# Optimization experiments

Hardware: AMD Instinct MI355X
Metric: run time of the kernel (lower is better)

The kernel has to match this reference:

```python
import jax, jax.numpy as jnp
import numpy as np

N, T, C, H = 512, 64, 64, 4
HD = C // H
FE = 4  # forward_expansion
EPS = 1e-5


def _p(key, shape, scale=0.05):
    return jax.random.normal(key, shape, dtype=jnp.float32) * scale


def setup_inputs() -> dict:
    key = jax.random.key(0)
    ks = jax.random.split(key, 24)
    return {
        'value': jax.random.normal(ks[0], (N, T, C), dtype=jnp.float32),
        'key_t': jax.random.normal(ks[1], (N, T, C), dtype=jnp.float32),
        'query': jax.random.normal(ks[2], (N, T, C), dtype=jnp.float32),
        'adj': jax.random.uniform(ks[3], (N, N), dtype=jnp.float32),
        # SSelfAttention params (nn.Linear weights, applied as x @ W.T)
        'Wv': _p(ks[4], (HD, HD)), 'Wk': _p(ks[5], (HD, HD)), 'Wq': _p(ks[6], (HD, HD)),
        'Wo': _p(ks[7], (C, C)), 'bo': jnp.zeros((C,), jnp.float32),
        # LayerNorms
        'g1': jnp.ones((C,), jnp.float32), 'b1': jnp.zeros((C,), jnp.float32),
        'g2': jnp.ones((C,), jnp.float32), 'b2': jnp.zeros((C,), jnp.float32),
        # FFN
        'Wf1': _p(ks[8], (FE * C, C)), 'bf1': jnp.zeros((FE * C,), jnp.float32),
        'Wf2': _p(ks[9], (C, FE * C)), 'bf2': jnp.zeros((C,), jnp.float32),
        # GCN (two GraphConvolution layers: adj @ (x @ W) + b, ReLU between)
        'Wg1': _p(ks[10], (C, C)), 'bg1': jnp.zeros((C,), jnp.float32),
        'Wg2': _p(ks[11], (C, C)), 'bg2': jnp.zeros((C,), jnp.float32),
        # gating linears
        'Wo1': _p(ks[12], (C, C)), 'bo1': jnp.zeros((C,), jnp.float32),
        'Wo2': _p(ks[13], (C, C)), 'bo2': jnp.zeros((C,), jnp.float32),
    }


def _layernorm(x, g, b):
    m = jnp.mean(x, axis=-1, keepdims=True)
    v = jnp.mean((x - m) ** 2, axis=-1, keepdims=True)
    return (x - m) * jax.lax.rsqrt(v + EPS) * g + b


def reference(value, key_t, query, adj, Wv, Wk, Wq, Wo, bo, g1, b1, g2, b2,
              Wf1, bf1, Wf2, bf2, Wg1, bg1, Wg2, bg2, Wo1, bo1, Wo2, bo2):
    n, t, c = query.shape
    # --- SSelfAttention: attention across nodes (q/k axes are nodes) ---
    vh = value.reshape(n, t, H, HD) @ Wv.T
    kh = key_t.reshape(n, t, H, HD) @ Wk.T
    qh = query.reshape(n, t, H, HD) @ Wq.T
    energy = jnp.einsum('qthd,kthd->qkth', qh, kh)  # [N,N,T,H]
    att = jax.nn.softmax(energy / jnp.sqrt(jnp.float32(c)), axis=1)
    attn_out = jnp.einsum('qkth,kthd->qthd', att, vh).reshape(n, t, c)
    attn_out = attn_out @ Wo.T + bo
    # --- residual + norm + FFN + norm (dropout = identity, eval mode) ---
    x = _layernorm(attn_out + query, g1, b1)
    ffn = jax.nn.relu(x @ Wf1.T + bf1) @ Wf2.T + bf2
    out1 = _layernorm(ffn + x, g2, b2)
    # --- InstanceNorm2d(1) on adj: normalize over whole NxN map (no affine) ---
    am = jnp.mean(adj)
    av = jnp.mean((adj - am) ** 2)
    adj_n = (adj - am) * jax.lax.rsqrt(av + EPS)
    # --- GCN applied per-timestep, vectorized over T ---
    h = jax.nn.relu(jnp.einsum('nm,mtc->ntc', adj_n, query @ Wg1.T) + bg1)
    out2 = jnp.einsum('nm,mtc->ntc', adj_n, h @ Wg2.T) + bg2
    # --- gated fusion ---
    g = jax.nn.sigmoid(out1 @ Wo1.T + bo1 + out2 @ Wo2.T + bo2)
    return g * out1 + (1.0 - g) * out2
```

## Files before the change

kernel.cpp:

```cpp
#include <hip/hip_runtime.h>

#define LN_EPS 1e-5f

typedef __attribute__((ext_vector_type(4))) short short4v;
typedef __attribute__((ext_vector_type(4))) float float4v;

__device__ __forceinline__ float wave_sum(float v) {
#pragma unroll
  for (int o = 32; o > 0; o >>= 1) v += __shfl_xor(v, o, 64);
  return v;
}

__device__ __forceinline__ unsigned short f2b(float f) {
  unsigned int u = __float_as_uint(f);
  u += 0x7fffu + ((u >> 16) & 1u);
  return (unsigned short)(u >> 16);
}

__device__ __forceinline__ float b2f(unsigned short h) {
  return __uint_as_float(((unsigned int)h) << 16);
}

__device__ __forceinline__ float4v mfma_16x16x16_bf16(short4v a, short4v b,
                                                      float4v c) {
#if __has_builtin(__builtin_amdgcn_mfma_f32_16x16x16bf16_1k)
  return __builtin_amdgcn_mfma_f32_16x16x16bf16_1k(a, b, c, 0, 0, 0);
#else
  float4v d;
  asm volatile(
      "v_mfma_f32_16x16x16_bf16 %0, %1, %2, %3\n\ts_nop 7\n\ts_nop 7"
      : "=v"(d)
      : "v"(a), "v"(b), "v"(c));
  return d;
#endif
}

__global__ __launch_bounds__(256) void s1_kernel(
    const float* __restrict__ adj, float* __restrict__ ps,
    float* __restrict__ pss, const float* __restrict__ value,
    const float* __restrict__ keyt, const float* __restrict__ query,
    const float* __restrict__ Wv, const float* __restrict__ Wk,
    const float* __restrict__ Wq, unsigned short* __restrict__ vt,
    unsigned short* __restrict__ kh, unsigned short* __restrict__ qh) {
  __shared__ float r1[4], r2[4];
  __shared__ __align__(16) float wv[256], wk[256], wq[256];
  const int b = blockIdx.x, tid = threadIdx.x;
  if (b < 512) {
    float v0 = adj[b * 512 + tid], v1 = adj[b * 512 + 256 + tid];
    float s = v0 + v1;
    float ss = fmaf(v0, v0, v1 * v1);
    s = wave_sum(s);
    ss = wave_sum(ss);
    if ((tid & 63) == 0) { r1[tid >> 6] = s; r2[tid >> 6] = ss; }
    __syncthreads();
    if (tid == 0) {
      ps[b] = r1[0] + r1[1] + r1[2] + r1[3];
      pss[b] = r2[0] + r2[1] + r2[2] + r2[3];
    }
  } else {
    wv[tid] = Wv[tid];
    wk[tid] = Wk[tid];
    wq[tid] = Wq[tid] * 0.125f;
    __syncthreads();
    const int th = b - 512;
    const int t = th >> 2, h = th & 3;
    const int base = t * 64 + h * 16;
    float y[16];
    unsigned short tmp[16];

#define XFORM(SRC, WARR)                                            \
  {                                                                 \
    const float4* p = (const float4*)(SRC + n * 4096 + base);       \
    float x[16];                                                    \
    *(float4*)(x + 0) = p[0];                                       \
    *(float4*)(x + 4) = p[1];                                       \
    *(float4*)(x + 8) = p[2];                                       \
    *(float4*)(x + 12) = p[3];                                      \
    _Pragma("unroll") for (int d = 0; d < 16; ++d) {                \
      float acc = 0.f;                                              \
      _Pragma("unroll") for (int e4 = 0; e4 < 4; ++e4) {            \
        float4 w4 = *(const float4*)&WARR[d * 16 + e4 * 4];         \
        acc = fmaf(w4.x, x[e4 * 4 + 0], acc);                       \
        acc = fmaf(w4.y, x[e4 * 4 + 1], acc);                       \
        acc = fmaf(w4.z, x[e4 * 4 + 2], acc);                       \
        acc = fmaf(w4.w, x[e4 * 4 + 3], acc);                       \
      }                                                             \
      y[d] = acc;                                                   \
    }                                                               \
  }

    for (int s = 0; s < 2; ++s) {
      const int n = tid + (s << 8);
      XFORM(value, wv)
#pragma unroll
      for (int d = 0; d < 16; ++d) vt[th * 8192 + d * 512 + n] = f2b(y[d]);
      XFORM(keyt, wk)
#pragma unroll
      for (int d = 0; d < 16; ++d) tmp[d] = f2b(y[d]);
      *(int4*)&kh[(th * 512 + n) * 16] = *(int4*)&tmp[0];
      *(int4*)&kh[(th * 512 + n) * 16 + 8] = *(int4*)&tmp[8];
      XFORM(query, wq)
#pragma unroll
      for (int d = 0; d < 16; ++d) tmp[d] = f2b(y[d]);
      *(int4*)&qh[(th * 512 + n) * 16] = *(int4*)&tmp[0];
      *(int4*)&qh[(th * 512 + n) * 16 + 8] = *(int4*)&tmp[8];
    }
#undef XFORM
  }
}

#define VPAD 536
__global__ __launch_bounds__(256) void s2_kernel(
    const float* __restrict__ adj, const float* __restrict__ ps,
    const float* __restrict__ pss, const float* __restrict__ query,
    const float* __restrict__ Wg1, const float* __restrict__ Wf1,
    const float* __restrict__ Wf2, const float* __restrict__ Wo1,
    const float* __restrict__ Wo2, const float* __restrict__ Wg2,
    const float* __restrict__ Wo, const float* __restrict__ bg2,
    const float* __restrict__ bo1, const float* __restrict__ bo2,
    unsigned short* __restrict__ anh, unsigned short* __restrict__ anl,
    unsigned short* __restrict__ Yfh, unsigned short* __restrict__ Yfl,
    unsigned short* __restrict__ Wf1f, unsigned short* __restrict__ Wf2f,
    unsigned short* __restrict__ Wo1f, unsigned short* __restrict__ Wg2hf,
    unsigned short* __restrict__ Wg2lf, unsigned short* __restrict__ W32hf,
    unsigned short* __restrict__ W32lf, unsigned short* __restrict__ Wof,
    float* __restrict__ c2, const unsigned short* __restrict__ qh,
    const unsigned short* __restrict__ kh, const unsigned short* __restrict__ vt,
    unsigned short* __restrict__ obf) {
  __shared__ float r1[4], r2[4];
  __shared__ __align__(16) char smem[33280];
  const int tid = threadIdx.x, b = blockIdx.x;
  if (b < 900) {
    float* pool = (float*)smem;
    if (b < 256) {
      float s = ps[tid] + ps[tid + 256];
      float ss = pss[tid] + pss[tid + 256];
      s = wave_sum(s);
      ss = wave_sum(ss);
      if ((tid & 63) == 0) { r1[tid >> 6] = s; r2[tid >> 6] = ss; }
      __syncthreads();
      const float sum = r1[0] + r1[1] + r1[2] + r1[3];
      const float sqs = r2[0] + r2[1] + r2[2] + r2[3];
      const float am = sum * (1.f / 262144.f);
      const float var = sqs * (1.f / 262144.f) - am * am;
      const float rs = rsqrtf(var + LN_EPS);
      const int i = (b * 256 + tid) * 4;
      float4 v = *(const float4*)&adj[i];
      float vals[4] = {(v.x - am) * rs, (v.y - am) * rs, (v.z - am) * rs,
                       (v.w - am) * rs};
      unsigned short th4[4], tl4[4];
#pragma unroll
      for (int j = 0; j < 4; ++j) {
        th4[j] = f2b(vals[j]);
        tl4[j] = f2b(vals[j] - b2f(th4[j]));
      }
      *(short4v*)&anh[i] = *(short4v*)th4;
      *(short4v*)&anl[i] = *(short4v*)tl4;
    } else if (b < 320) {
      const int id = (b - 256) * 256 + tid;
      const int n = id >> 6, k = id & 63;
      Wf1f[((k >> 4) * 256 + n) * 16 + (k & 15)] = f2b(Wf1[id]);
    } else if (b < 384) {
      const int id = (b - 320) * 256 + tid;
      const int n = id >> 8, k = id & 255;
      Wf2f[((k >> 4) * 64 + n) * 16 + (k & 15)] = f2b(Wf2[id]);
    } else if (b < 896) {
      const int pb = b - 384;
      const int w = tid >> 6, lane = tid & 63;
      const int mt = pb & 31;
      const int t = (pb >> 5) * 4 + w;
      float* xs = pool;
      float* Ls = pool + 256;
      float wc[64];
#pragma unroll
      for (int e = 0; e < 16; ++e)
        *(float4*)&wc[e * 4] = *(const float4*)&Wg1[lane * 64 + e * 4];
#pragma unroll 4
      for (int ms = 0; ms < 16; ++ms) {
        const int r = (mt * 16 + ms) * 64 + t;
        xs[w * 64 + lane] = query[r * 64 + lane];
        float acc = 0.f;
#pragma unroll
        for (int e = 0; e < 64; ++e) acc = fmaf(xs[w * 64 + e], wc[e], acc);
        Ls[(w * 16 + ms) * 68 + lane] = acc;
      }
      unsigned int dh[8], dl[8];
#pragma unroll
      for (int j = 0; j < 8; ++j) {
        float v0 = Ls[(w * 16 + 2 * j) * 68 + lane];
        float v1 = Ls[(w * 16 + 2 * j + 1) * 68 + lane];
        unsigned int h0 = f2b(v0), h1 = f2b(v1);
        unsigned int l0 = f2b(v0 - b2f((unsigned short)h0));
        unsigned int l1 = f2b(v1 - b2f((unsigned short)h1));
        dh[j] = h0 | (h1 << 16);
        dl[j] = l0 | (l1 << 16);
      }
      const int off = ((mt * 4096) + t * 64 + lane) * 16;
      *(uint4*)(Yfh + off) = *(uint4*)&dh[0];
      *(uint4*)(Yfh + off + 8) = *(uint4*)&dh[4];
      *(uint4*)(Yfl + off) = *(uint4*)&dl[0];
      *(uint4*)(Yfl + off + 8) = *(uint4*)&dl[4];
    } else if (b == 896) {
      for (int i = tid; i < 4096; i += 256) {
        const int n = i >> 6, k = i & 63;
        Wo1f[((k >> 4) * 64 + n) * 16 + (k & 15)] = f2b(Wo1[i]);
      }
    } else if (b == 897) {
      for (int i = tid; i < 4096; i += 256) {
        const int n = i >> 6, k = i & 63;
        const float v = Wg2[i];
        const unsigned short h = f2b(v);
        const unsigned short l = f2b(v - b2f(h));
        Wg2hf[((k >> 4) * 64 + n) * 16 + (k & 15)] = h;
        Wg2lf[((k >> 4) * 64 + n) * 16 + (k & 15)] = l;
      }
    } else if (b == 898) {
      float* wo2s = pool;
      float* wg2s = pool + 4096;
      float* bg2s = pool + 8192;
      for (int i = tid; i < 4096; i += 256) {
        wo2s[i] = Wo2[i];
        wg2s[i] = Wg2[i];
      }
      if (tid < 64) bg2s[tid] = bg2[tid];
      __syncthreads();
#pragma unroll 4
      for (int t = 0; t < 16; ++t) {
        const int i = t * 256 + tid;
        const int r = i >> 6, c = i & 63;
        float acc = 0.f;
#pragma unroll
        for (int e = 0; e < 64; ++e)
          acc = fmaf(wo2s[r * 64 + e], wg2s[e * 64 + c], acc);
        const unsigned short h = f2b(acc);
        const unsigned short l = f2b(acc - b2f(h));
        W32hf[((c >> 4) * 64 + r) * 16 + (c & 15)] = h;
        W32lf[((c >> 4) * 64 + r) * 16 + (c & 15)] = l;
      }
      if (tid < 64) {
        float acc = bo1[tid] + bo2[tid];
#pragma unroll
        for (int e = 0; e < 64; ++e)
          acc = fmaf(wo2s[tid * 64 + e], bg2s[e], acc);
        c2[tid] = acc;
      }
    } else {
      for (int i = tid; i < 4096; i += 256) {
        const int n = i >> 6, k = i & 63;
        Wof[((k >> 4) * 64 + n) * 16 + (k & 15)] = f2b(Wo[i]);
      }
    }
  } else {
    unsigned short* Vs = (unsigned short*)smem;
    const int bx = b - 900;
    const int th = bx >> 2;
    {
      const unsigned short* vb = vt + th * 8192;
#pragma unroll
      for (int it = 0; it < 4; ++it) {
        const int flat = (it * 256 + tid) * 8;
        const int d = flat >> 9, k = flat & 511;
        *(int4*)&Vs[d * VPAD + k] = *(const int4*)&vb[flat];
      }
    }
    __syncthreads();

    const int lane = tid & 15;
    const int quad = (tid >> 4) & 3;
    const int w = tid >> 6;
    const int q0 = (bx & 3) * 128 + w * 32;

    const unsigned short* qbase = qh + th * 8192;
    const unsigned short* kbase = kh + th * 8192;
    short4v qf[2];
#pragma unroll
    for (int ct = 0; ct < 2; ++ct)
      qf[ct] = *(const short4v*)&qbase[(q0 + ct * 16 + lane) * 16 + quad * 4];

    float4v acc[2];
    float l[2];
#pragma unroll
    for (int ct = 0; ct < 2; ++ct) {
      acc[ct].x = 0.f; acc[ct].y = 0.f; acc[ct].z = 0.f; acc[ct].w = 0.f;
      l[ct] = 0.f;
    }
    float4v zero;
    zero.x = 0.f; zero.y = 0.f; zero.z = 0.f; zero.w = 0.f;

    const unsigned short* vrow = &Vs[lane * VPAD];

    for (int kt = 0; kt < 32; ++kt) {
      const short4v kf =
          *(const short4v*)&kbase[(kt * 16 + lane) * 16 + quad * 4];
      const short4v vf = *(const short4v*)&vrow[kt * 16 + quad * 4];
#pragma unroll
      for (int ct = 0; ct < 2; ++ct) {
        float4v s = mfma_16x16x16_bf16(kf, qf[ct], zero);
        float p0 = __expf(s.x);
        float p1 = __expf(s.y);
        float p2 = __expf(s.z);
        float p3 = __expf(s.w);
        l[ct] += (p0 + p1) + (p2 + p3);
        unsigned int u0 = __float_as_uint(p0) + 0x8000u;
        unsigned int u1 = __float_as_uint(p1) + 0x8000u;
        unsigned int u2 = __float_as_uint(p2) + 0x8000u;
        unsigned int u3 = __float_as_uint(p3) + 0x8000u;
        union {
          uint2 u;
          short4v s4;
        } pk;
        pk.u.x = __builtin_amdgcn_perm(u1, u0, 0x07060302u);
        pk.u.y = __builtin_amdgcn_perm(u3, u2, 0x07060302u);
        acc[ct] = mfma_16x16x16_bf16(vf, pk.s4, acc[ct]);
      }
    }

    const int t = th >> 2, h = th & 3;
#pragma unroll
    for (int ct = 0; ct < 2; ++ct) {
      float lt = l[ct];
      lt += __shfl_xor(lt, 16, 64);
      lt += __shfl_xor(lt, 32, 64);
      const float inv = 1.f / lt;
      unsigned short tmp[4];
      tmp[0] = f2b(acc[ct].x * inv);
      tmp[1] = f2b(acc[ct].y * inv);
      tmp[2] = f2b(acc[ct].z * inv);
      tmp[3] = f2b(acc[ct].w * inv);
      const int q = q0 + ct * 16 + lane;
      *(uint2*)&obf[(q * 64 + t) * 64 + h * 16 + quad * 4] = *(uint2*)tmp;
    }
  }
}

__global__ __launch_bounds__(256) void s3_kernel(
    const unsigned short* __restrict__ obf, const float* __restrict__ query,
    const unsigned short* __restrict__ Wof, const float* __restrict__ bo,
    const float* __restrict__ g1, const float* __restrict__ b1,
    const unsigned short* __restrict__ Wf1f, const float* __restrict__ bf1,
    const unsigned short* __restrict__ Wf2f, const float* __restrict__ bf2,
    const float* __restrict__ g2, const float* __restrict__ b2,
    float* __restrict__ out1, unsigned short* __restrict__ out1b,
    const unsigned short* __restrict__ Ah, const unsigned short* __restrict__ Al,
    const unsigned short* __restrict__ Bh, const unsigned short* __restrict__ Bl,
    const float* __restrict__ bg1, unsigned short* __restrict__ Hh,
    unsigned short* __restrict__ Hl) {
  __shared__ __align__(16) char smem[41984];
  const int tid = threadIdx.x, b = blockIdx.x;
  const int w = tid >> 6, lane = tid & 63;
  const int ln = lane & 15, quad = lane >> 4;
  if (b < 512) {
    unsigned short* xb = (unsigned short*)smem;
    unsigned short* hid = (unsigned short*)(smem + 8704);
    const int n = b;
    float xres[4][4];

    {
      const unsigned short* ap = obf + (n * 64 + w * 16 + ln) * 64 + quad * 4;
      float4v acc[4];
#pragma unroll
      for (int j = 0; j < 4; ++j) {
        acc[j].x = 0.f; acc[j].y = 0.f; acc[j].z = 0.f; acc[j].w = 0.f;
      }
#pragma unroll
      for (int kt = 0; kt < 4; ++kt) {
        const short4v a = *(const short4v*)(ap + kt * 16);
#pragma unroll
        for (int j = 0; j < 4; ++j) {
          const short4v bfr =
              *(const short4v*)&Wof[(kt * 64 + j * 16 + ln) * 16 + quad * 4];
          acc[j] = mfma_16x16x16_bf16(a, bfr, acc[j]);
        }
      }
#pragma unroll
      for (int reg = 0; reg < 4; ++reg) {
        const int row = w * 16 + quad * 4 + reg;
        float v[4];
        float s = 0.f;
#pragma unroll
        for (int j = 0; j < 4; ++j) {
          const int col = j * 16 + ln;
          v[j] = acc[j][reg] + bo[col] + query[(n * 64 + row) * 64 + col];
          s += v[j];
        }
        s += __shfl_xor(s, 1, 64);
        s += __shfl_xor(s, 2, 64);
        s += __shfl_xor(s, 4, 64);
        s += __shfl_xor(s, 8, 64);
        const float mean = s * 0.015625f;
        float vv = 0.f;
#pragma unroll
        for (int j = 0; j < 4; ++j) {
          const float dd = v[j] - mean;
          vv += dd * dd;
        }
        vv += __shfl_xor(vv, 1, 64);
        vv += __shfl_xor(vv, 2, 64);
        vv += __shfl_xor(vv, 4, 64);
        vv += __shfl_xor(vv, 8, 64);
        const float rs = rsqrtf(vv * 0.015625f + LN_EPS);
#pragma unroll
        for (int j = 0; j < 4; ++j) {
          const int col = j * 16 + ln;
          const float xv = (v[j] - mean) * rs * g1[col] + b1[col];
          xres[j][reg] = xv;
          xb[row * 68 + col] = f2b(xv);
        }
      }
    }
    __syncthreads();

    {
      const int wm = (w & 1) * 32, wn = (w >> 1) * 128;
      float4v acc[2][8];
#pragma unroll
      for (int i = 0; i < 2; ++i)
#pragma unroll
        for (int j = 0; j < 8; ++j) {
          acc[i][j].x = 0.f; acc[i][j].y = 0.f;
          acc[i][j].z = 0.f; acc[i][j].w = 0.f;
        }
#pragma unroll
      for (int kt = 0; kt < 4; ++kt) {
        short4v a0 = *(const short4v*)&xb[(wm + ln) * 68 + kt * 16 + quad * 4];
        short4v a1 =
            *(const short4v*)&xb[(wm + 16 + ln) * 68 + kt * 16 + quad * 4];
#pragma unroll
        for (int j = 0; j < 8; ++j) {
          short4v bfr = *(const short4v*)&Wf1f[(kt * 256 + wn + j * 16 + ln) *
                                                   16 + quad * 4];
          acc[0][j] = mfma_16x16x16_bf16(a0, bfr, acc[0][j]);
          acc[1][j] = mfma_16x16x16_bf16(a1, bfr, acc[1][j]);
        }
      }
#pragma unroll
      for (int mt = 0; mt < 2; ++mt)
#pragma unroll
        for (int j = 0; j < 8; ++j) {
          const int col = wn + j * 16 + ln;
          const float bb = bf1[col];
#pragma unroll
          for (int reg = 0; reg < 4; ++reg) {
            const int row = wm + mt * 16 + quad * 4 + reg;
            hid[row * 260 + col] = f2b(fmaxf(acc[mt][j][reg] + bb, 0.f));
          }
        }
    }
    __syncthreads();

    {
      float4v acc[4];
#pragma unroll
      for (int j = 0; j < 4; ++j) {
        acc[j].x = 0.f; acc[j].y = 0.f; acc[j].z = 0.f; acc[j].w = 0.f;
      }
#pragma unroll 4
      for (int kt = 0; kt < 16; ++kt) {
        short4v a =
            *(const short4v*)&hid[(w * 16 + ln) * 260 + kt * 16 + quad * 4];
#pragma unroll
        for (int j = 0; j < 4; ++j) {
          short4v bfr =
              *(const short4v*)&Wf2f[(kt * 64 + j * 16 + ln) * 16 + quad * 4];
          acc[j] = mfma_16x16x16_bf16(a, bfr, acc[j]);
        }
      }
#pragma unroll
      for (int reg = 0; reg < 4; ++reg) {
        const int row = w * 16 + quad * 4 + reg;
        float v[4];
        float s = 0.f;
#pragma unroll
        for (int j = 0; j < 4; ++j) {
          v[j] = acc[j][reg] + bf2[j * 16 + ln] + xres[j][reg];
          s += v[j];
        }
        s += __shfl_xor(s, 1, 64);
        s += __shfl_xor(s, 2, 64);
        s += __shfl_xor(s, 4, 64);
        s += __shfl_xor(s, 8, 64);
        const float mean = s * 0.015625f;
        float vv = 0.f;
#pragma unroll
        for (int j = 0; j < 4; ++j) {
          const float dd = v[j] - mean;
          vv += dd * dd;
        }
        vv += __shfl_xor(vv, 1, 64);
        vv += __shfl_xor(vv, 2, 64);
        vv += __shfl_xor(vv, 4, 64);
        vv += __shfl_xor(vv, 8, 64);
        const float rs = rsqrtf(vv * 0.015625f + LN_EPS);
#pragma unroll
        for (int j = 0; j < 4; ++j) {
          const float ov =
              (v[j] - mean) * rs * g2[j * 16 + ln] + b2[j * 16 + ln];
          const int idx = (n * 64 + row) * 64 + j * 16 + ln;
          out1[idx] = ov;
          out1b[idx] = f2b(ov);
        }
      }
    }
  } else {
    const int pb = b - 512;
    const int wave = w;
    const int wm = (wave & 1) * 32, wn = (wave >> 1) * 64;
    const int m0 = (pb >> 5) * 64 + wm;
    const int n0 = (pb & 31) * 128 + wn;

    const unsigned short* ah0 = Ah + (m0 + ln) * 512 + quad * 4;
    const unsigned short* al0 = Al + (m0 + ln) * 512 + quad * 4;
    const unsigned short* bh0 = Bh + (n0 + ln) * 16 + quad * 4;
    const unsigned short* bl0 = Bl + (n0 + ln) * 16 + quad * 4;

    float4v acc[2][4];
#pragma unroll
    for (int i = 0; i < 2; ++i)
#pragma unroll
      for (int j = 0; j < 4; ++j) {
        acc[i][j].x = 0.f; acc[i][j].y = 0.f;
        acc[i][j].z = 0.f; acc[i][j].w = 0.f;
      }

#pragma unroll 2
    for (int kt = 0; kt < 32; ++kt) {
      short4v a0h = *(const short4v*)(ah0 + kt * 16);
      short4v a1h = *(const short4v*)(ah0 + 16 * 512 + kt * 16);
      short4v a0l = *(const short4v*)(al0 + kt * 16);
      short4v a1l = *(const short4v*)(al0 + 16 * 512 + kt * 16);
#pragma unroll
      for (int j = 0; j < 4; ++j) {
        const int boff = (kt * 4096 + j * 16) * 16;
        short4v bh = *(const short4v*)(bh0 + boff);
        short4v bl = *(const short4v*)(bl0 + boff);
        acc[0][j] = mfma_16x16x16_bf16(a0l, bh, acc[0][j]);
        acc[0][j] = mfma_16x16x16_bf16(a0h, bl, acc[0][j]);
        acc[0][j] = mfma_16x16x16_bf16(a0h, bh, acc[0][j]);
        acc[1][j] = mfma_16x16x16_bf16(a1l, bh, acc[1][j]);
        acc[1][j] = mfma_16x16x16_bf16(a1h, bl, acc[1][j]);
        acc[1][j] = mfma_16x16x16_bf16(a1h, bh, acc[1][j]);
      }
    }

#pragma unroll
    for (int mt = 0; mt < 2; ++mt) {
      const int mtile = (m0 + mt * 16) >> 4;
#pragma unroll
      for (int j = 0; j < 4; ++j) {
        const int col = n0 + j * 16 + ln;
        const float bb = bg1[col & 63];
        unsigned short hh[4], hl[4];
#pragma unroll
        for (int reg = 0; reg < 4; ++reg) {
          float v = fmaxf(acc[mt][j][reg] + bb, 0.f);
          hh[reg] = f2b(v);
          hl[reg] = f2b(v - b2f(hh[reg]));
        }
        const int off = (mtile * 4096 + col) * 16 + quad * 4;
        *(uint2*)&Hh[off] = *(uint2*)hh;
        *(uint2*)&Hl[off] = *(uint2*)hl;
      }
    }
  }
}

__global__ __launch_bounds__(256) void s4_kernel(
    const unsigned short* __restrict__ Ah, const unsigned short* __restrict__ Al,
    const unsigned short* __restrict__ Bh, const unsigned short* __restrict__ Bl,
    unsigned short* __restrict__ G2h, unsigned short* __restrict__ G2l) {
  const int tid = threadIdx.x;
  const int wave = tid >> 6, lane = tid & 63;
  const int ln = lane & 15, quad = lane >> 4;
  const int wm = (wave & 1) * 32, wn = (wave >> 1) * 32;
  const int m0 = (blockIdx.x >> 6) * 64 + wm;
  const int n0 = (blockIdx.x & 63) * 64 + wn;

  const unsigned short* ah0 = Ah + (m0 + ln) * 512 + quad * 4;
  const unsigned short* al0 = Al + (m0 + ln) * 512 + quad * 4;
  const unsigned short* bh0 = Bh + (n0 + ln) * 16 + quad * 4;
  const unsigned short* bl0 = Bl + (n0 + ln) * 16 + quad * 4;

  float4v acc[2][2];
#pragma unroll
  for (int i = 0; i < 2; ++i)
#pragma unroll
    for (int j = 0; j < 2; ++j) {
      acc[i][j].x = 0.f; acc[i][j].y = 0.f;
      acc[i][j].z = 0.f; acc[i][j].w = 0.f;
    }

#pragma unroll 4
  for (int kt = 0; kt < 32; ++kt) {
    short4v a0h = *(const short4v*)(ah0 + kt * 16);
    short4v a1h = *(const short4v*)(ah0 + 16 * 512 + kt * 16);
    short4v a0l = *(const short4v*)(al0 + kt * 16);
    short4v a1l = *(const short4v*)(al0 + 16 * 512 + kt * 16);
#pragma unroll
    for (int j = 0; j < 2; ++j) {
      const int boff = (kt * 4096 + j * 16) * 16;
      short4v bh = *(const short4v*)(bh0 + boff);
      short4v bl = *(const short4v*)(bl0 + boff);
      acc[0][j] = mfma_16x16x16_bf16(a0l, bh, acc[0][j]);
      acc[0][j] = mfma_16x16x16_bf16(a0h, bl, acc[0][j]);
      acc[0][j] = mfma_16x16x16_bf16(a0h, bh, acc[0][j]);
      acc[1][j] = mfma_16x16x16_bf16(a1l, bh, acc[1][j]);
      acc[1][j] = mfma_16x16x16_bf16(a1h, bl, acc[1][j]);
      acc[1][j] = mfma_16x16x16_bf16(a1h, bh, acc[1][j]);
    }
  }

#pragma unroll
  for (int mt = 0; mt < 2; ++mt)
#pragma unroll
    for (int j = 0; j < 2; ++j) {
      const int col = n0 + j * 16 + ln;
#pragma unroll
      for (int reg = 0; reg < 4; ++reg) {
        const int row = m0 + mt * 16 + quad * 4 + reg;
        const float v = acc[mt][j][reg];
        const unsigned short h = f2b(v);
        G2h[row * 4096 + col] = h;
        G2l[row * 4096 + col] = f2b(v - b2f(h));
      }
    }
}

__global__ __launch_bounds__(256) void s5_kernel(
    const unsigned short* __restrict__ out1b, const float* __restrict__ out1,
    const unsigned short* __restrict__ G2h, const unsigned short* __restrict__ G2l,
    const unsigned short* __restrict__ Wo1f, const unsigned short* __restrict__ Wg2hf,
    const unsigned short* __restrict__ Wg2lf, const unsigned short* __restrict__ W32hf,
    const unsigned short* __restrict__ W32lf, const float* __restrict__ bg2,
    const float* __restrict__ c2, float* __restrict__ dst) {
  const int tid = threadIdx.x;
  const int wave = tid >> 6, lane = tid & 63;
  const int ln = lane & 15, quad = lane >> 4;
  const int m0 = blockIdx.x * 64 + wave * 16;

  const unsigned short* o1p = out1b + (m0 + ln) * 64 + quad * 4;
  const unsigned short* ghp = G2h + (m0 + ln) * 64 + quad * 4;
  const unsigned short* glp = G2l + (m0 + ln) * 64 + quad * 4;

  float4v aco[4], aca[4];
#pragma unroll
  for (int j = 0; j < 4; ++j) {
    aco[j].x = 0.f; aco[j].y = 0.f; aco[j].z = 0.f; aco[j].w = 0.f;
    aca[j].x = 0.f; aca[j].y = 0.f; aca[j].z = 0.f; aca[j].w = 0.f;
  }

#pragma unroll
  for (int kt = 0; kt < 4; ++kt) {
    const short4v ao = *(const short4v*)(o1p + kt * 16);
    const short4v gh = *(const short4v*)(ghp + kt * 16);
    const short4v gl = *(const short4v*)(glp + kt * 16);
#pragma unroll
    for (int j = 0; j < 4; ++j) {
      const int boff = (kt * 64 + j * 16 + ln) * 16 + quad * 4;
      const short4v wgh = *(const short4v*)(Wg2hf + boff);
      const short4v wgl = *(const short4v*)(Wg2lf + boff);
      const short4v wo1 = *(const short4v*)(Wo1f + boff);
      const short4v w3h = *(const short4v*)(W32hf + boff);
      const short4v w3l = *(const short4v*)(W32lf + boff);
      aco[j] = mfma_16x16x16_bf16(gl, wgh, aco[j]);
      aco[j] = mfma_16x16x16_bf16(gh, wgl, aco[j]);
      aco[j] = mfma_16x16x16_bf16(gh, wgh, aco[j]);
      aca[j] = mfma_16x16x16_bf16(ao, wo1, aca[j]);
      aca[j] = mfma_16x16x16_bf16(gl, w3h, aca[j]);
      aca[j] = mfma_16x16x16_bf16(gh, w3l, aca[j]);
      aca[j] = mfma_16x16x16_bf16(gh, w3h, aca[j]);
    }
  }

#pragma unroll
  for (int j = 0; j < 4; ++j) {
    const int col = j * 16 + ln;
    const float bg2v = bg2[col];
    const float c2v = c2[col];
#pragma unroll
    for (int reg = 0; reg < 4; ++reg) {
      const int row = m0 + quad * 4 + reg;
      const float o2 = aco[j][reg] + bg2v;
      const float a = aca[j][reg] + c2v;
      const float o1v = out1[row * 64 + col];
      const float g = 1.f / (1.f + __expf(-a));
      dst[row * 64 + col] = o2 + g * (o1v - o2);
    }
  }
}

extern "C" void kernel_launch(void* const* d_in, const int* in_sizes, int n_in,
                              void* d_out, int out_size, void* d_ws,
                              size_t ws_size, hipStream_t stream) {
  const float* value = (const float*)d_in[0];
  const float* key_t = (const float*)d_in[1];
  const float* query = (const float*)d_in[2];
  const float* adj = (const float*)d_in[3];
  const float* Wv = (const float*)d_in[4];
  const float* Wk = (const float*)d_in[5];
  const float* Wq = (const float*)d_in[6];
  const float* Wo = (const float*)d_in[7];
  const float* bo = (const float*)d_in[8];
  const float* g1 = (const float*)d_in[9];
  const float* b1 = (const float*)d_in[10];
  const float* g2 = (const float*)d_in[11];
  const float* b2 = (const float*)d_in[12];
  const float* Wf1 = (const float*)d_in[13];
  const float* bf1 = (const float*)d_in[14];
  const float* Wf2 = (const float*)d_in[15];
  const float* bf2 = (const float*)d_in[16];
  const float* Wg1 = (const float*)d_in[17];
  const float* bg1 = (const float*)d_in[18];
  const float* Wg2 = (const float*)d_in[19];
  const float* bg2 = (const float*)d_in[20];
  const float* Wo1 = (const float*)d_in[21];
  const float* bo1 = (const float*)d_in[22];
  const float* Wo2 = (const float*)d_in[23];
  const float* bo2 = (const float*)d_in[24];

  float* ws = (float*)d_ws;
  const size_t M1 = 1048576;
  unsigned short* obf = (unsigned short*)(ws + 0);
  float* out1 = ws + 2 * M1;
  unsigned short* out1b = (unsigned short*)(ws + 4 * M1);
  unsigned short* qh = (unsigned short*)(ws + 5 * M1);
  unsigned short* kh = (unsigned short*)(ws + 6 * M1);
  unsigned short* vt = (unsigned short*)(ws + 7 * M1);
  unsigned short* Yfh = (unsigned short*)(ws + 8 * M1);
  unsigned short* Yfl = (unsigned short*)(ws + 9 * M1);
  unsigned short* Hrfh = (unsigned short*)(ws + 10 * M1);
  unsigned short* Hrfl = (unsigned short*)(ws + 11 * M1);
  unsigned short* G2h = (unsigned short*)(ws + 12 * M1);
  unsigned short* G2l = (unsigned short*)(ws + 13 * M1);
  unsigned short* anh = (unsigned short*)(ws + 14 * M1);
  unsigned short* anl = (unsigned short*)(ws + 14 * M1 + 131072);
  float* wbase = ws + 14 * M1 + 262144;
  unsigned short* Wf1f = (unsigned short*)(wbase);
  unsigned short* Wf2f = (unsigned short*)(wbase + 8192);
  unsigned short* Wo1f = (unsigned short*)(wbase + 16384);
  unsigned short* Wg2hf = (unsigned short*)(wbase + 18432);
  unsigned short* Wg2lf = (unsigned short*)(wbase + 20480);
  unsigned short* W32hf = (unsigned short*)(wbase + 22528);
  unsigned short* W32lf = (unsigned short*)(wbase + 24576);
  unsigned short* Wof = (unsigned short*)(wbase + 26624);
  float* c2 = wbase + 28672;
  float* ps = wbase + 28736;
  float* pss = ps + 512;
  float* dst = (float*)d_out;

  s1_kernel<<<768, 256, 0, stream>>>(adj, ps, pss, value, key_t, query, Wv,
                                     Wk, Wq, vt, kh, qh);
  s2_kernel<<<1924, 256, 0, stream>>>(adj, ps, pss, query, Wg1, Wf1, Wf2, Wo1,
                                      Wo2, Wg2, Wo, bg2, bo1, bo2, anh, anl,
                                      Yfh, Yfl, Wf1f, Wf2f, Wo1f, Wg2hf,
                                      Wg2lf, W32hf, W32lf, Wof, c2, qh, kh,
                                      vt, obf);
  s3_kernel<<<768, 256, 0, stream>>>(obf, query, Wof, bo, g1, b1, Wf1f, bf1,
                                     Wf2f, bf2, g2, b2, out1, out1b, anh, anl,
                                     Yfh, Yfl, bg1, Hrfh, Hrfl);
  s4_kernel<<<512, 256, 0, stream>>>(anh, anl, Hrfh, Hrfl, G2h, G2l);
  s5_kernel<<<512, 256, 0, stream>>>(out1b, out1, G2h, G2l, Wo1f, Wg2hf,
                                     Wg2lf, W32hf, W32lf, bg2, c2, dst);
}
```

Before: 253.0 us.

## Fuse GCN second aggregation with gated-fusion epilogue through shared memory

Merges the adjacency-aggregation GEMM (s4) and the gating/output kernel (s5) into one kernel. The aggregated tile stays in LDS instead of being written to global memory as hi/lo bf16 pairs and read back, which also removes one launch. The three split-precision products now go into separate accumulators so the MFMA chains are independent, at the cost of more registers. Each block now covers one timestep for 64 nodes, so the out1/dst accesses are strided by timestep.

```diff
diff --git a/kernel.cpp b/kernel.cpp
--- a/kernel.cpp
+++ b/kernel.cpp
@@ -564,126 +564,134 @@
   }
 }
 
-__global__ __launch_bounds__(256) void s4_kernel(
+__global__ __launch_bounds__(256) void s45_kernel(
     const unsigned short* __restrict__ Ah, const unsigned short* __restrict__ Al,
     const unsigned short* __restrict__ Bh, const unsigned short* __restrict__ Bl,
-    unsigned short* __restrict__ G2h, unsigned short* __restrict__ G2l) {
-  const int tid = threadIdx.x;
-  const int wave = tid >> 6, lane = tid & 63;
-  const int ln = lane & 15, quad = lane >> 4;
-  const int wm = (wave & 1) * 32, wn = (wave >> 1) * 32;
-  const int m0 = (blockIdx.x >> 6) * 64 + wm;
-  const int n0 = (blockIdx.x & 63) * 64 + wn;
-
-  const unsigned short* ah0 = Ah + (m0 + ln) * 512 + quad * 4;
-  const unsigned short* al0 = Al + (m0 + ln) * 512 + quad * 4;
-  const unsigned short* bh0 = Bh + (n0 + ln) * 16 + quad * 4;
-  const unsigned short* bl0 = Bl + (n0 + ln) * 16 + quad * 4;
-
-  float4v acc[2][2];
-#pragma unroll
-  for (int i = 0; i < 2; ++i)
-#pragma unroll
-    for (int j = 0; j < 2; ++j) {
-      acc[i][j].x = 0.f; acc[i][j].y = 0.f;
-      acc[i][j].z = 0.f; acc[i][j].w = 0.f;
-    }
-
-#pragma unroll 4
-  for (int kt = 0; kt < 32; ++kt) {
-    short4v a0h = *(const short4v*)(ah0 + kt * 16);
-    short4v a1h = *(const short4v*)(ah0 + 16 * 512 + kt * 16);
-    short4v a0l = *(const short4v*)(al0 + kt * 16);
-    short4v a1l = *(const short4v*)(al0 + 16 * 512 + kt * 16);
-#pragma unroll
-    for (int j = 0; j < 2; ++j) {
-      const int boff = (kt * 4096 + j * 16) * 16;
-      short4v bh = *(const short4v*)(bh0 + boff);
-      short4v bl = *(const short4v*)(bl0 + boff);
-      acc[0][j] = mfma_16x16x16_bf16(a0l, bh, acc[0][j]);
-      acc[0][j] = mfma_16x16x16_bf16(a0h, bl, acc[0][j]);
-      acc[0][j] = mfma_16x16x16_bf16(a0h, bh, acc[0][j]);
-      acc[1][j] = mfma_16x16x16_bf16(a1l, bh, acc[1][j]);
-      acc[1][j] = mfma_16x16x16_bf16(a1h, bl, acc[1][j]);
-      acc[1][j] = mfma_16x16x16_bf16(a1h, bh, acc[1][j]);
-    }
-  }
-
-#pragma unroll
-  for (int mt = 0; mt < 2; ++mt)
-#pragma unroll
-    for (int j = 0; j < 2; ++j) {
-      const int col = n0 + j * 16 + ln;
-#pragma unroll
-      for (int reg = 0; reg < 4; ++reg) {
-        const int row = m0 + mt * 16 + quad * 4 + reg;
-        const float v = acc[mt][j][reg];
-        const unsigned short h = f2b(v);
-        G2h[row * 4096 + col] = h;
-        G2l[row * 4096 + col] = f2b(v - b2f(h));
-      }
-    }
-}
-
-__global__ __launch_bounds__(256) void s5_kernel(
     const unsigned short* __restrict__ out1b, const float* __restrict__ out1,
-    const unsigned short* __restrict__ G2h, const unsigned short* __restrict__ G2l,
     const unsigned short* __restrict__ Wo1f, const unsigned short* __restrict__ Wg2hf,
     const unsigned short* __restrict__ Wg2lf, const unsigned short* __restrict__ W32hf,
     const unsigned short* __restrict__ W32lf, const float* __restrict__ bg2,
     const float* __restrict__ c2, float* __restrict__ dst) {
+  __shared__ __align__(16) float Ls[64 * 68];
   const int tid = threadIdx.x;
   const int wave = tid >> 6, lane = tid & 63;
   const int ln = lane & 15, quad = lane >> 4;
-  const int m0 = blockIdx.x * 64 + wave * 16;
-
-  const unsigned short* o1p = out1b + (m0 + ln) * 64 + quad * 4;
-  const unsigned short* ghp = G2h + (m0 + ln) * 64 + quad * 4;
-  const unsigned short* glp = G2l + (m0 + ln) * 64 + quad * 4;
-
-  float4v aco[4], aca[4];
-#pragma unroll
-  for (int j = 0; j < 4; ++j) {
-    aco[j].x = 0.f; aco[j].y = 0.f; aco[j].z = 0.f; aco[j].w = 0.f;
-    aca[j].x = 0.f; aca[j].y = 0.f; aca[j].z = 0.f; aca[j].w = 0.f;
+  const int N0 = (blockIdx.x >> 6) * 64;
+  const int t = blockIdx.x & 63;
+
+  {
+    const int wm = (wave & 1) * 32, wn = (wave >> 1) * 32;
+    const int m0 = N0 + wm;
+    const int n0 = t * 64 + wn;
+    const unsigned short* ah0 = Ah + (m0 + ln) * 512 + quad * 4;
+    const unsigned short* al0 = Al + (m0 + ln) * 512 + quad * 4;
+    const unsigned short* bh0 = Bh + (n0 + ln) * 16 + quad * 4;
+    const unsigned short* bl0 = Bl + (n0 + ln) * 16 + quad * 4;
+
+    float4v ahh[2][2], ahl[2][2], alh[2][2];
+#pragma unroll
+    for (int i = 0; i < 2; ++i)
+#pragma unroll
+      for (int j = 0; j < 2; ++j) {
+        ahh[i][j].x = 0.f; ahh[i][j].y = 0.f;
+        ahh[i][j].z = 0.f; ahh[i][j].w = 0.f;
+        ahl[i][j] = ahh[i][j];
+        alh[i][j] = ahh[i][j];
+      }
+
+#pragma unroll 4
+    for (int kt = 0; kt < 32; ++kt) {
+      short4v a0h = *(const short4v*)(ah0 + kt * 16);
+      short4v a1h = *(const short4v*)(ah0 + 16 * 512 + kt * 16);
+      short4v a0l = *(const short4v*)(al0 + kt * 16);
+      short4v a1l = *(const short4v*)(al0 + 16 * 512 + kt * 16);
+#pragma unroll
+      for (int j = 0; j < 2; ++j) {
+        const int boff = (kt * 4096 + j * 16) * 16;
+        short4v bh = *(const short4v*)(bh0 + boff);
+        short4v bl = *(const short4v*)(bl0 + boff);
+        ahh[0][j] = mfma_16x16x16_bf16(a0h, bh, ahh[0][j]);
+        ahl[0][j] = mfma_16x16x16_bf16(a0h, bl, ahl[0][j]);
+        alh[0][j] = mfma_16x16x16_bf16(a0l, bh, alh[0][j]);
+        ahh[1][j] = mfma_16x16x16_bf16(a1h, bh, ahh[1][j]);
+        ahl[1][j] = mfma_16x16x16_bf16(a1h, bl, ahl[1][j]);
+        alh[1][j] = mfma_16x16x16_bf16(a1l, bh, alh[1][j]);
+      }
+    }
+
+#pragma unroll
+    for (int mt = 0; mt < 2; ++mt)
+#pragma unroll
+      for (int j = 0; j < 2; ++j) {
+        const int c = wn + j * 16 + ln;
+#pragma unroll
+        for (int reg = 0; reg < 4; ++reg) {
+          const int r = wm + mt * 16 + quad * 4 + reg;
+          Ls[r * 68 + c] =
+              ahh[mt][j][reg] + ahl[mt][j][reg] + alh[mt][j][reg];
+        }
+      }
   }
-
-#pragma unroll
-  for (int kt = 0; kt < 4; ++kt) {
-    const short4v ao = *(const short4v*)(o1p + kt * 16);
-    const short4v gh = *(const short4v*)(ghp + kt * 16);
-    const short4v gl = *(const short4v*)(glp + kt * 16);
+  __syncthreads();
+
+  {
+    const int rloc = wave * 16;
+    float4v aco[4], aca[4];
 #pragma unroll
     for (int j = 0; j < 4; ++j) {
-      const int boff = (kt * 64 + j * 16 + ln) * 16 + quad * 4;
-      const short4v wgh = *(const short4v*)(Wg2hf + boff);
-      const short4v wgl = *(const short4v*)(Wg2lf + boff);
-      const short4v wo1 = *(const short4v*)(Wo1f + boff);
-      const short4v w3h = *(const short4v*)(W32hf + boff);
-      const short4v w3l = *(const short4v*)(W32lf + boff);
-      aco[j] = mfma_16x16x16_bf16(gl, wgh, aco[j]);
-      aco[j] = mfma_16x16x16_bf16(gh, wgl, aco[j]);
-      aco[j] = mfma_16x16x16_bf16(gh, wgh, aco[j]);
-      aca[j] = mfma_16x16x16_bf16(ao, wo1, aca[j]);
-      aca[j] = mfma_16x16x16_bf16(gl, w3h, aca[j]);
-      aca[j] = mfma_16x16x16_bf16(gh, w3l, aca[j]);
-      aca[j] = mfma_16x16x16_bf16(gh, w3h, aca[j]);
-    }
-  }
-
-#pragma unroll
-  for (int j = 0; j < 4; ++j) {
-    const int col = j * 16 + ln;
-    const float bg2v = bg2[col];
-    const float c2v = c2[col];
-#pragma unroll
-    for (int reg = 0; reg < 4; ++reg) {
-      const int row = m0 + quad * 4 + reg;
-      const float o2 = aco[j][reg] + bg2v;
-      const float a = aca[j][reg] + c2v;
-      const float o1v = out1[row * 64 + col];
-      const float g = 1.f / (1.f + __expf(-a));
-      dst[row * 64 + col] = o2 + g * (o1v - o2);
+      aco[j].x = 0.f; aco[j].y = 0.f; aco[j].z = 0.f; aco[j].w = 0.f;
+      aca[j].x = 0.f; aca[j].y = 0.f; aca[j].z = 0.f; aca[j].w = 0.f;
+    }
+    const unsigned short* o1p =
+        out1b + ((N0 + rloc + ln) * 64 + t) * 64 + quad * 4;
+
+#pragma unroll
+    for (int kt = 0; kt < 4; ++kt) {
+      float4 gv = *(const float4*)&Ls[(rloc + ln) * 68 + kt * 16 + quad * 4];
+      unsigned short ghv[4], glv[4];
+      {
+        const float g4[4] = {gv.x, gv.y, gv.z, gv.w};
+#pragma unroll
+        for (int e = 0; e < 4; ++e) {
+          ghv[e] = f2b(g4[e]);
+          glv[e] = f2b(g4[e] - b2f(ghv[e]));
+        }
+      }
+      const short4v gh = *(short4v*)ghv;
+      const short4v gl = *(short4v*)glv;
+      const short4v ao = *(const short4v*)(o1p + kt * 16);
+#pragma unroll
+      for (int j = 0; j < 4; ++j) {
+        const int boff = (kt * 64 + j * 16 + ln) * 16 + quad * 4;
+        const short4v wgh = *(const short4v*)(Wg2hf + boff);
+        const short4v wgl = *(const short4v*)(Wg2lf + boff);
+        const short4v wo1 = *(const short4v*)(Wo1f + boff);
+        const short4v w3h = *(const short4v*)(W32hf + boff);
+        const short4v w3l = *(const short4v*)(W32lf + boff);
+        aco[j] = mfma_16x16x16_bf16(gl, wgh, aco[j]);
+        aco[j] = mfma_16x16x16_bf16(gh, wgl, aco[j]);
+        aco[j] = mfma_16x16x16_bf16(gh, wgh, aco[j]);
+        aca[j] = mfma_16x16x16_bf16(ao, wo1, aca[j]);
+        aca[j] = mfma_16x16x16_bf16(gl, w3h, aca[j]);
+        aca[j] = mfma_16x16x16_bf16(gh, w3l, aca[j]);
+        aca[j] = mfma_16x16x16_bf16(gh, w3h, aca[j]);
+      }
+    }
+
+#pragma unroll
+    for (int j = 0; j < 4; ++j) {
+      const int col = j * 16 + ln;
+      const float bg2v = bg2[col];
+      const float c2v = c2[col];
+#pragma unroll
+      for (int reg = 0; reg < 4; ++reg) {
+        const int rowg = (N0 + rloc + quad * 4 + reg) * 64 + t;
+        const float o2 = aco[j][reg] + bg2v;
+        const float a = aca[j][reg] + c2v;
+        const float o1v = out1[rowg * 64 + col];
+        const float g = 1.f / (1.f + __expf(-a));
+        dst[rowg * 64 + col] = o2 + g * (o1v - o2);
+      }
     }
   }
 }
@@ -729,8 +737,6 @@
   unsigned short* Yfl = (unsigned short*)(ws + 9 * M1);
   unsigned short* Hrfh = (unsigned short*)(ws + 10 * M1);
   unsigned short* Hrfl = (unsigned short*)(ws + 11 * M1);
-  unsigned short* G2h = (unsigned short*)(ws + 12 * M1);
-  unsigned short* G2l = (unsigned short*)(ws + 13 * M1);
   unsigned short* anh = (unsigned short*)(ws + 14 * M1);
   unsigned short* anl = (unsigned short*)(ws + 14 * M1 + 131072);
   float* wbase = ws + 14 * M1 + 262144;
@@ -757,7 +763,7 @@
   s3_kernel<<<768, 256, 0, stream>>>(obf, query, Wof, bo, g1, b1, Wf1f, bf1,
                                      Wf2f, bf2, g2, b2, out1, out1b, anh, anl,
                                      Yfh, Yfl, bg1, Hrfh, Hrfl);
-  s4_kernel<<<512, 256, 0, stream>>>(anh, anl, Hrfh, Hrfl, G2h, G2l);
-  s5_kernel<<<512, 256, 0, stream>>>(out1b, out1, G2h, G2l, Wo1f, Wg2hf,
-                                     Wg2lf, W32hf, W32lf, bg2, c2, dst);
-}
+  s45_kernel<<<512, 256, 0, stream>>>(anh, anl, Hrfh, Hrfl, out1b, out1,
+                                      Wo1f, Wg2hf, Wg2lf, W32hf, W32lf, bg2,
+                                      c2, dst);
+}
```

Measured after the change: 246.8 us. 2.4% less time.
